# Kernel tuning notes

Hardware: AMD Instinct MI355X
Metric: run time of the kernel (lower is better)

The kernel has to match this reference:

```python
import jax, jax.numpy as jnp
import numpy as np

HEADS, DH, DIM = 16, 64, 1024
GAMMA, LAMBDA_REG = 0.01, 0.001


def _ln(x, g, b, eps=1e-5):
    mu = x.mean(-1, keepdims=True)
    var = x.var(-1, keepdims=True)  # biased var, matches torch LayerNorm
    return (x - mu) / jnp.sqrt(var + eps) * g + b


def setup_inputs() -> dict:
    key = jax.random.key(0)
    ks = jax.random.split(key, 8)
    B, NQ, NK = 8, 512, 512
    inner = HEADS * DH
    rn = lambda i, shp, sc: jax.random.normal(ks[i], shp, jnp.float32) * sc
    return {
        "q": rn(0, (B, NQ, DIM), 1.0),
        "k": rn(1, (B, NK, DIM), 1.0),
        "v": rn(2, (B, NK, DIM), 1.0),
        "ln_g": jnp.ones((DIM,), jnp.float32),
        "ln_b": jnp.zeros((DIM,), jnp.float32),
        "w_in": rn(3, (DIM, inner), 0.02),
        "wp_w1": rn(4, (2 * DH, DH), 0.05),
        "wp_b1": jnp.zeros((DH,), jnp.float32),
        "wp_lng": jnp.ones((DH,), jnp.float32),
        "wp_lnb": jnp.zeros((DH,), jnp.float32),
        "wp_w2": rn(5, (DH, DH // 2), 0.05),
        "wp_b2": jnp.zeros((DH // 2,), jnp.float32),
        "wp_w3": rn(6, (DH // 2, 3), 0.05),
        "wp_b3": jnp.zeros((3,), jnp.float32),
        "w_temp": jnp.ones((1,), jnp.float32) * 0.8,
        "w_out": rn(7, (inner, DIM), 0.02),
        "b_out": jnp.zeros((DIM,), jnp.float32),
    }


def reference(q, k, v, ln_g, ln_b, w_in, wp_w1, wp_b1, wp_lng, wp_lnb,
              wp_w2, wp_b2, wp_w3, wp_b3, w_temp, w_out, b_out):
    sg = jax.lax.stop_gradient

    def proj(x):  # input_linear (dropout=identity in eval) + head split
        y = _ln(x, ln_g, ln_b) @ w_in                      # [B,N,inner]
        B, N, _ = y.shape
        return y.reshape(B, N, HEADS, DH).transpose(2, 0, 1, 3)  # [h,B,N,d]

    f_q, f_k, f_v = proj(q), proj(k), proj(v)
    m = f_k.shape[2]
    eps = 1e-8

    # --- cosine component (clamp applied twice, as in source) ---
    dots = jnp.einsum('hbnd,hbmd->hbnm', f_q, f_k)
    n1 = jnp.linalg.norm(f_q, axis=-1, keepdims=True) + eps   # [h,B,Nq,1]
    n2 = jnp.linalg.norm(f_k, axis=-1, keepdims=True) + eps   # [h,B,Nk,1]
    cosine_sim = jnp.clip(dots / (n1 * jnp.swapaxes(n2, -1, -2)), -0.98, 0.98)

    # --- regularized covariance component ---
    f_kc = f_k - f_k.mean(axis=2, keepdims=True)
    f_qc = f_q - f_q.mean(axis=-1, keepdims=True)
    cov = jnp.einsum('hbnd,hbmd->hbnm', f_qc, f_kc) / (DH ** 0.5 + 1e-6)
    health = jnp.std(cov, ddof=1)
    base = LAMBDA_REG / max(m, 1)
    reg = jnp.where(health < 1e-5, base * 5.0,
                    jnp.where(health < 1e-3, base * 2.0, base))
    cov = jnp.clip(reg * cov, -25.0, 25.0)

    # --- margin-based variance component (eval: adaptive_gamma = gamma) ---
    fqn = f_q / jnp.maximum(jnp.linalg.norm(f_q, axis=-1, keepdims=True), 1e-6)
    fkn = f_k / jnp.maximum(jnp.linalg.norm(f_k, axis=-1, keepdims=True), 1e-6)
    cs = jnp.clip(jnp.einsum('hbnd,hbmd->hbnm', fqn, fkn), -0.98, 0.98)
    margin = jnp.clip(GAMMA - cs, 0.0, 5.0)
    var_c = jnp.broadcast_to(margin.mean(-1, keepdims=True), cs.shape)

    # --- dynamic per-head weight predictor MLP ---
    qk = jnp.concatenate([f_q.mean(axis=(1, 2)), f_k.mean(axis=(1, 2))], -1)  # [h,2d]
    h1 = jax.nn.relu(_ln(qk @ wp_w1 + wp_b1, wp_lng, wp_lnb))
    h2 = jax.nn.relu(h1 @ wp_w2 + wp_b2)
    logits = jax.nn.softmax(h2 @ wp_w3 + wp_b3, -1)  # MLP ends in Softmax
    temp = jnp.clip(w_temp, 0.1, 5.0)
    w = jax.nn.softmax(logits / temp, -1)            # second softmax with temp
    w = jnp.clip(w, 0.08, 0.75)
    w = w / w.sum(-1, keepdims=True)
    cw = w[:, 0].reshape(HEADS, 1, 1, 1)
    covw = w[:, 1].reshape(HEADS, 1, 1, 1)
    varw = w[:, 2].reshape(HEADS, 1, 1, 1)

    # --- health-based normalization (stds detached, as in source) ---
    cn = sg(jnp.std(cosine_sim, ddof=1)) + 1e-6
    covn = sg(jnp.std(cov, ddof=1)) + 1e-6
    varn = sg(jnp.std(var_c, ddof=1)) + 1e-6
    ch = jnp.minimum(cn, 1.0)
    covh = jnp.minimum(covn * 10.0, 1.0)
    varh = jnp.minimum(varn * 10.0, 1.0)
    dots_f = (cw * (cosine_sim / cn * ch)
              + covw * (cov / covn * 0.4 * covh)
              + varw * (var_c / varn * 0.4 * varh))

    # --- diversity-adaptive softmax temperature ---
    div = jnp.std(dots_f, ddof=1)
    atemp = jnp.where(div < 1e-5, 0.05, jnp.where(div < 1e-3, 0.2, 0.5 + div))
    atemp = jnp.clip(atemp, 0.05, 2.0)
    attn = jax.nn.softmax(dots_f / atemp, axis=-1)

    out = jnp.einsum('hbnm,hbmd->hbnd', attn, f_v)
    out = out.transpose(1, 2, 0, 3).reshape(q.shape[0], q.shape[1], HEADS * DH)
    return out @ w_out + b_out  # output_linear (dropout=identity)
```

## Files before the change

kernel.cpp:

```cpp
#include <hip/hip_runtime.h>
#include <math.h>

#define NHEADS 16
#define DHEAD  64
#define NDIM   1024
#define NB     8
#define NSEQ   512
#define NROWS  4096
#define NHB    128
#define NTOTD  33554432.0

typedef __bf16 bf16x8 __attribute__((ext_vector_type(8)));
typedef __bf16 bf16x4 __attribute__((ext_vector_type(4)));
typedef float  f32x4  __attribute__((ext_vector_type(4)));

#define MFMA(a,b,c) __builtin_amdgcn_mfma_f32_16x16x32_bf16(a,b,c,0,0,0)

static __device__ __forceinline__ size_t qk_off(int hbq, int n, int d){
  return ((size_t)hbq*32 + (n>>4))*1024 + (size_t)(d>>3)*128 + (size_t)(n&15)*8 + (d&7);
}
static __device__ __forceinline__ size_t fr_off(int r, int k2, int kblocks8){
  return ((size_t)(r>>4)*kblocks8 + (k2>>3))*128 + (size_t)(r&15)*8 + (k2&7);
}

#define O_DSUMH  0
#define O_DSUME  1024
#define O_SCAL   2048
#define O_COEF   3072
#define O_W      4096
#define O_RQ1    131072
#define O_RQ2    393216
#define O_MQ     655360
#define O_QDMK   917504
#define O_RK1    1179648
#define O_RK2    1441792
#define O_KS2    1703936
#define O_MARG   1966080
#define O_RCS    2228224
#define O_RCOV   2490368
#define O_MK     2752512
#define O_QCOL   2785280
#define O_QHI    4194304
#define O_QLO    12582912
#define O_KHI    20971520
#define O_KLO    29360128
#define O_VTH    37748736
#define O_VTL    46137344
#define O_LNST   54525952
#define O_WTH    71303168
#define O_WTL    73400320
#define O_OUTH   75497472
#define O_OUTL   83886080
#define O_WOTH   92274688
#define O_WOTL   94371840

static __device__ __forceinline__ float clamp98(float x){ return fminf(fmaxf(x,-0.98f),0.98f); }

__global__ __launch_bounds__(256) void ln_stats_kernel(const float* __restrict__ q,
    const float* __restrict__ k, const float* __restrict__ v, float* __restrict__ st){
  int row = blockIdx.x, t = threadIdx.x;
  const float* x = (blockIdx.y==0) ? q : (blockIdx.y==1 ? k : v);
  float4 vv = *(const float4*)(x + (size_t)row*1024 + t*4);
  float s  = vv.x+vv.y+vv.z+vv.w;
  float ss = vv.x*vv.x+vv.y*vv.y+vv.z*vv.z+vv.w*vv.w;
  for (int off=32; off; off>>=1){ s += __shfl_down(s,off); ss += __shfl_down(ss,off); }
  __shared__ float sh[8];
  if ((t&63)==0){ sh[t>>6]=s; sh[4+(t>>6)]=ss; }
  __syncthreads();
  if (t==0){
    float S=sh[0]+sh[1]+sh[2]+sh[3], SS=sh[4]+sh[5]+sh[6]+sh[7];
    float mu = S*(1.0f/1024.0f);
    st[blockIdx.y*8192 + row*2]   = mu;
    st[blockIdx.y*8192 + row*2+1] = 1.0f/sqrtf(SS*(1.0f/1024.0f) - mu*mu + 1e-5f);
  }
}

__global__ __launch_bounds__(256) void transpose_split_kernel(const float* __restrict__ wsrc,
    __bf16* __restrict__ th, __bf16* __restrict__ tl){
  __shared__ float tile[64][65];
  int k0 = blockIdx.x*64, n0 = blockIdx.y*64;
  int t = threadIdx.x;
  int c = t&63, r4 = t>>6;
  #pragma unroll
  for (int i=0;i<16;i++){
    int kr = r4 + i*4;
    tile[kr][c] = wsrc[(size_t)(k0+kr)*1024 + n0 + c];
  }
  __syncthreads();
  #pragma unroll
  for (int i=0;i<16;i++){
    int nr = r4 + i*4;
    float v = tile[c][nr];
    __bf16 hv = (__bf16)v;
    size_t o = fr_off(n0+nr, k0+c, 128);
    th[o] = hv; tl[o] = (__bf16)(v - (float)hv);
  }
}

__global__ __launch_bounds__(256,4) void proj_gemm_kernel(
  const float* __restrict__ q, const float* __restrict__ k, const float* __restrict__ v,
  const float* __restrict__ lnst0,
  const float* __restrict__ gv, const float* __restrict__ bv,
  const __bf16* __restrict__ Bth, const __bf16* __restrict__ Btl,
  __bf16* __restrict__ qhi, __bf16* __restrict__ qlo,
  __bf16* __restrict__ khi, __bf16* __restrict__ klo,
  __bf16* __restrict__ vth, __bf16* __restrict__ vtl)
{
  __shared__ __bf16 Ash[128][72];
  __shared__ __bf16 Asl[128][72];
  int z = blockIdx.z;
  const float* X = (z==0)? q : (z==1? k : v);
  const float* lnst = lnst0 + z*8192;
  __bf16* oh = (z==0)? qhi : (z==1? khi : vth);
  __bf16* ol = (z==0)? qlo : (z==1? klo : vtl);
  int t = threadIdx.x, w = t>>6, lane = t&63, lr = lane&15, lq = lane>>4;
  int vid = blockIdx.y*16 + blockIdx.x;
  int cX = vid&7, r2 = vid>>3;
  int ytile = cX*4 + (r2>>4);
  int xtile = r2&15;
  int rbase = ytile*128;
  int cbase = xtile*64;
  int wr = w>>1, wc = w&1;
  int srow = t>>3;
  int scol = (t&7)*8;
  int cb16_0 = (cbase + wc*32)>>4;
  f32x4 acc[4][2] = {};
  for (int kt=0; kt<16; kt++){
    int k0 = kt*64;
    bf16x8 va[4], vA[4];
    float4 g0 = *(const float4*)(gv + k0 + scol);
    float4 g1 = *(const float4*)(gv + k0 + scol + 4);
    float4 b0 = *(const float4*)(bv + k0 + scol);
    float4 b1 = *(const float4*)(bv + k0 + scol + 4);
    #pragma unroll
    for (int r=0;r<4;r++){
      int row = rbase + r*32 + srow;
      size_t gi = (size_t)row*1024 + k0 + scol;
      float4 x0 = *(const float4*)(X + gi);
      float4 x1 = *(const float4*)(X + gi + 4);
      float mu = lnst[row*2], rs = lnst[row*2+1];
      float o[8];
      o[0]=(x0.x-mu)*rs*g0.x+b0.x; o[1]=(x0.y-mu)*rs*g0.y+b0.y;
      o[2]=(x0.z-mu)*rs*g0.z+b0.z; o[3]=(x0.w-mu)*rs*g0.w+b0.w;
      o[4]=(x1.x-mu)*rs*g1.x+b1.x; o[5]=(x1.y-mu)*rs*g1.y+b1.y;
      o[6]=(x1.z-mu)*rs*g1.z+b1.z; o[7]=(x1.w-mu)*rs*g1.w+b1.w;
      bf16x8 hv, lv;
      #pragma unroll
      for (int e=0;e<8;e++){
        __bf16 hb_ = (__bf16)o[e];
        hv[e] = hb_; lv[e] = (__bf16)(o[e]-(float)hb_);
      }
      va[r]=hv; vA[r]=lv;
    }
    #pragma unroll
    for (int r=0;r<4;r++){
      *(bf16x8*)&Ash[r*32+srow][scol] = va[r];
      *(bf16x8*)&Asl[r*32+srow][scol] = vA[r];
    }
    __syncthreads();
    #pragma unroll
    for (int kc=0; kc<2; kc++){
      int ko = kc*32 + lq*8;
      bf16x8 ah[4], al[4], bh[2], bl[2];
      #pragma unroll
      for (int i=0;i<4;i++){
        ah[i] = *(const bf16x8*)&Ash[wr*64 + i*16 + lr][ko];
        al[i] = *(const bf16x8*)&Asl[wr*64 + i*16 + lr][ko];
      }
      #pragma unroll
      for (int j=0;j<2;j++){
        size_t bo = ((size_t)(cb16_0+j)*128 + (k0>>3) + kc*4)*128 + (size_t)lane*8;
        bh[j] = *(const bf16x8*)(Bth + bo);
        bl[j] = *(const bf16x8*)(Btl + bo);
      }
      #pragma unroll
      for (int i=0;i<4;i++)
        #pragma unroll
        for (int j=0;j<2;j++){
          acc[i][j] = MFMA(al[i], bh[j], acc[i][j]);
          acc[i][j] = MFMA(ah[i], bl[j], acc[i][j]);
          acc[i][j] = MFMA(ah[i], bh[j], acc[i][j]);
        }
    }
    __syncthreads();
  }
  #pragma unroll
  for (int i=0;i<4;i++)
    #pragma unroll
    for (int j=0;j<2;j++)
      #pragma unroll
      for (int r=0;r<4;r++){
        int row = rbase + wr*64 + i*16 + lq*4 + r;
        int col = cbase + wc*32 + j*16 + lr;
        float val = acc[i][j][r];
        __bf16 hv = (__bf16)val;
        __bf16 lv = (__bf16)(val - (float)hv);
        int n = row & 511, b2 = row >> 9;
        int hh = col >> 6, d = col & 63;
        int hbq = hh*8 + b2;
        size_t o;
        if (z<2){
          o = qk_off(hbq, n, d);
        } else {
          o = (((size_t)hbq*4 + (d>>4))*16 + (n>>5))*512
            + (size_t)((((n>>3)&3)*16) + (d&15))*8 + (n&7);
        }
        oh[o] = hv; ol[o] = lv;
      }
}

__global__ __launch_bounds__(256) void final_gemm_kernel(
  const __bf16* __restrict__ Ah, const __bf16* __restrict__ Al,
  const __bf16* __restrict__ Bth, const __bf16* __restrict__ Btl,
  const float* __restrict__ bias, float* __restrict__ of)
{
  int t = threadIdx.x, w = t>>6, lane = t&63, lr = lane&15, lq = lane>>4;
  int vid = blockIdx.y*16 + blockIdx.x;
  int cX = vid&7, r2 = vid>>3;
  int ytile = cX*4 + (r2>>4);
  int xtile = r2&15;
  int rbase = ytile*128;
  int cbase = xtile*64;
  int wr = w>>1, wc = w&1;
  int rb16_0 = (rbase + wr*64)>>4;
  int cb16_0 = (cbase + wc*32)>>4;
  f32x4 acc[4][2] = {};
  for (int ks=0; ks<32; ks++){
    int kb = ks*4;
    bf16x8 ah[4], al[4], bh[2], bl[2];
    #pragma unroll
    for (int i=0;i<4;i++){
      size_t ao = ((size_t)(rb16_0+i)*128 + kb)*128 + (size_t)lane*8;
      ah[i] = *(const bf16x8*)(Ah + ao);
      al[i] = *(const bf16x8*)(Al + ao);
    }
    #pragma unroll
    for (int j=0;j<2;j++){
      size_t bo = ((size_t)(cb16_0+j)*128 + kb)*128 + (size_t)lane*8;
      bh[j] = *(const bf16x8*)(Bth + bo);
      bl[j] = *(const bf16x8*)(Btl + bo);
    }
    #pragma unroll
    for (int i=0;i<4;i++)
      #pragma unroll
      for (int j=0;j<2;j++){
        acc[i][j] = MFMA(al[i], bh[j], acc[i][j]);
        acc[i][j] = MFMA(ah[i], bl[j], acc[i][j]);
        acc[i][j] = MFMA(ah[i], bh[j], acc[i][j]);
      }
  }
  #pragma unroll
  for (int i=0;i<4;i++)
    #pragma unroll
    for (int j=0;j<2;j++)
      #pragma unroll
      for (int r=0;r<4;r++){
        int row = rbase + wr*64 + i*16 + lq*4 + r;
        int col = cbase + wc*32 + j*16 + lr;
        of[(size_t)row*1024 + col] = acc[i][j][r] + bias[col];
      }
}

__global__ void kstats_kernel(const __bf16* __restrict__ kh, const __bf16* __restrict__ kl,
    float* __restrict__ mk, float* __restrict__ rk1, float* __restrict__ rk2, float* __restrict__ ks2){
  int hb = blockIdx.x;
  size_t base = (size_t)hb*32768;
  int t = threadIdx.x;
  __shared__ float csA[32][64];
  __shared__ float mks_lds[64];
  __shared__ float mksum_sh;
  int c2 = t&7, mg = t>>3;
  float fs[8] = {};
  for (int m=mg; m<512; m+=32){
    size_t off = base + (size_t)(m>>4)*1024 + c2*128 + (size_t)(m&15)*8;
    bf16x8 h = *(const bf16x8*)(kh+off);
    bf16x8 l = *(const bf16x8*)(kl+off);
    #pragma unroll
    for (int e=0;e<8;e++) fs[e] += (float)h[e]+(float)l[e];
  }
  #pragma unroll
  for (int e=0;e<8;e++) csA[mg][c2*8+e] = fs[e];
  __syncthreads();
  if (t<64){
    float s=0;
    #pragma unroll
    for (int g=0;g<32;g++) s += csA[g][t];
    float vv = s*(1.0f/512.0f);
    mk[hb*64+t] = vv;
    mks_lds[t] = vv;
  }
  __syncthreads();
  if (t==0){
    float s=0;
    for (int i=0;i<64;i++) s += mks_lds[i];
    mksum_sh = s;
  }
  __syncthreads();
  float mks = mksum_sh;
  int l8 = t&7, rg = t>>3;
  for (int m=rg; m<512; m+=32){
    size_t off = base + (size_t)(m>>4)*1024 + l8*128 + (size_t)(m&15)*8;
    bf16x8 h = *(const bf16x8*)(kh+off);
    bf16x8 l = *(const bf16x8*)(kl+off);
    float s=0, ss=0;
    #pragma unroll
    for (int e=0;e<8;e++){ float vv=(float)h[e]+(float)l[e]; s+=vv; ss+=vv*vv; }
    for (int o2=4;o2;o2>>=1){ s+=__shfl_xor(s,o2); ss+=__shfl_xor(ss,o2); }
    if (l8==0){
      float nk = sqrtf(ss);
      rk1[hb*512+m] = 1.0f/(nk+1e-8f);
      rk2[hb*512+m] = 1.0f/fmaxf(nk,1e-6f);
      ks2[hb*512+m] = s - mks;
    }
  }
}

__global__ void qstats_kernel(const __bf16* __restrict__ qh, const __bf16* __restrict__ ql,
    const float* __restrict__ mk, float* __restrict__ rq1, float* __restrict__ rq2,
    float* __restrict__ mq, float* __restrict__ qdotmk, float* __restrict__ qcol){
  int hb = blockIdx.x;
  size_t base = (size_t)hb*32768;
  int t = threadIdx.x;
  __shared__ float csA[32][64];
  __shared__ float mks_lds[64];
  int c2 = t&7, mg = t>>3;
  if (t<64) mks_lds[t] = mk[hb*64+t];
  float fs[8] = {};
  for (int m=mg; m<512; m+=32){
    size_t off = base + (size_t)(m>>4)*1024 + c2*128 + (size_t)(m&15)*8;
    bf16x8 h = *(const bf16x8*)(qh+off);
    bf16x8 l = *(const bf16x8*)(ql+off);
    #pragma unroll
    for (int e=0;e<8;e++) fs[e] += (float)h[e]+(float)l[e];
  }
  #pragma unroll
  for (int e=0;e<8;e++) csA[mg][c2*8+e] = fs[e];
  __syncthreads();
  if (t<64){
    float s=0;
    #pragma unroll
    for (int g=0;g<32;g++) s += csA[g][t];
    qcol[hb*64+t] = s;
  }
  int l8 = t&7, rg = t>>3;
  float mkv[8];
  #pragma unroll
  for (int e=0;e<8;e++) mkv[e] = mks_lds[l8*8+e];
  for (int n=rg; n<512; n+=32){
    size_t off = base + (size_t)(n>>4)*1024 + l8*128 + (size_t)(n&15)*8;
    bf16x8 h = *(const bf16x8*)(qh+off);
    bf16x8 l = *(const bf16x8*)(ql+off);
    float s=0, ss=0, qd=0;
    #pragma unroll
    for (int e=0;e<8;e++){
      float vv=(float)h[e]+(float)l[e];
      s+=vv; ss+=vv*vv; qd+=vv*mkv[e];
    }
    for (int o2=4;o2;o2>>=1){ s+=__shfl_xor(s,o2); ss+=__shfl_xor(ss,o2); qd+=__shfl_xor(qd,o2); }
    if (l8==0){
      float nq = sqrtf(ss);
      rq1[hb*512+n] = 1.0f/(nq+1e-8f);
      rq2[hb*512+n] = 1.0f/fmaxf(nq,1e-6f);
      mq[hb*512+n]  = s*(1.0f/64.0f);
      qdotmk[hb*512+n] = qd;
    }
  }
}

__global__ void mlp_kernel(const float* __restrict__ qcol, const float* __restrict__ mk,
   const float* __restrict__ w1, const float* __restrict__ b1, const float* __restrict__ lng,
   const float* __restrict__ lnb, const float* __restrict__ w2, const float* __restrict__ b2,
   const float* __restrict__ w3, const float* __restrict__ b3, const float* __restrict__ wtemp,
   float* __restrict__ W){
  int h = blockIdx.x;
  int j = threadIdx.x;
  __shared__ float qk[128], h1[64], h2[32];
  float sq=0, sk=0;
  #pragma unroll
  for (int b=0;b<8;b++){
    sq += qcol[(h*8+b)*64 + j];
    sk += mk[(h*8+b)*64 + j];
  }
  qk[j]    = sq*(1.0f/4096.0f);
  qk[64+j] = sk*(1.0f/8.0f);
  __syncthreads();
  float a = b1[j];
  for (int i=0;i<128;i++) a += qk[i]*w1[i*64+j];
  float s=a, ss=a*a;
  for (int off=32; off; off>>=1){ s += __shfl_xor(s,off); ss += __shfl_xor(ss,off); }
  float mu = s*(1.0f/64.0f), var = ss*(1.0f/64.0f)-mu*mu;
  float v = (a-mu)/sqrtf(var+1e-5f)*lng[j] + lnb[j];
  h1[j] = fmaxf(v, 0.0f);
  __syncthreads();
  if (j<32){
    float a2 = b2[j];
    for (int i=0;i<64;i++) a2 += h1[i]*w2[i*32+j];
    h2[j] = fmaxf(a2,0.0f);
  }
  __syncthreads();
  if (j==0){
    float l[3];
    for (int kq=0;kq<3;kq++){ float a3=b3[kq]; for(int i=0;i<32;i++) a3 += h2[i]*w3[i*3+kq]; l[kq]=a3; }
    float m = fmaxf(l[0],fmaxf(l[1],l[2]));
    float e0=expf(l[0]-m), e1=expf(l[1]-m), e2=expf(l[2]-m);
    float si = 1.0f/(e0+e1+e2);
    float temp = fminf(fmaxf(wtemp[0], 0.1f), 5.0f);
    float t0=e0*si/temp, t1=e1*si/temp, t2=e2*si/temp;
    float m2 = fmaxf(t0,fmaxf(t1,t2));
    float f0=expf(t0-m2), f1=expf(t1-m2), f2=expf(t2-m2);
    float s2i = 1.0f/(f0+f1+f2);
    float wv[3] = {f0*s2i, f1*s2i, f2*s2i};
    float wsum=0.0f;
    for (int kq=0;kq<3;kq++){ wv[kq]=fminf(fmaxf(wv[kq],0.08f),0.75f); wsum+=wv[kq]; }
    for (int kq=0;kq<3;kq++) W[h*3+kq] = wv[kq]/wsum;
  }
}

__global__ __launch_bounds__(256) void s1_mfma_kernel(
  const __bf16* __restrict__ qhp, const __bf16* __restrict__ qlp,
  const __bf16* __restrict__ khp, const __bf16* __restrict__ klp,
  const float* __restrict__ rq1, const float* __restrict__ rq2,
  const float* __restrict__ mq, const float* __restrict__ qdmk,
  const float* __restrict__ rk1, const float* __restrict__ rk2,
  const float* __restrict__ ks2,
  double* __restrict__ dsumH, float* __restrict__ margin,
  float* __restrict__ rcs, float* __restrict__ rcov)
{
  int vid = blockIdx.y*4 + blockIdx.x;
  int cX = vid&7, r2 = vid>>3;
  int hb = cX*16 + (r2>>2);
  int n0 = (r2&3)*128;
  size_t qb = (size_t)hb*32768;
  __shared__ float sm[512][3];
  __shared__ float sn[128][4];
  int t = threadIdx.x;
  for (int mm=t; mm<512; mm+=256){
    int m = hb*512 + mm;
    sm[mm][0]=rk1[m]; sm[mm][1]=rk2[m]; sm[mm][2]=ks2[m];
  }
  if (t<128){
    int n = hb*512 + n0 + t;
    sn[t][0]=rq1[n]; sn[t][1]=rq2[n]; sn[t][2]=mq[n]; sn[t][3]=qdmk[n];
  }
  __syncthreads();
  int w = t>>6, lane = t&63, lr = lane&15, lq = lane>>4;
  int nw = w*32;
  float lcs=0,lcs2=0,lcov=0,lcov2=0,lcscov=0;
  float mrow[2][4]={}, csr[2][4]={}, cvr[2][4]={};
  for (int mc=0; mc<4; mc++){
    int m0 = mc*128;
    f32x4 acc[2][8] = {};
    #pragma unroll
    for (int kc=0; kc<2; kc++){
      bf16x8 ah[2], al[2];
      #pragma unroll
      for (int i=0;i<2;i++){
        size_t off = qb + (size_t)(((n0+nw)>>4)+i)*1024 + kc*512 + (size_t)lane*8;
        ah[i] = *(const bf16x8*)(qhp + off);
        al[i] = *(const bf16x8*)(qlp + off);
      }
      #pragma unroll
      for (int j=0;j<8;j++){
        size_t off = qb + (size_t)((m0>>4)+j)*1024 + kc*512 + (size_t)lane*8;
        bf16x8 bh = *(const bf16x8*)(khp + off);
        bf16x8 bl = *(const bf16x8*)(klp + off);
        #pragma unroll
        for (int i=0;i<2;i++){
          acc[i][j] = MFMA(ah[i], bh, acc[i][j]);
          acc[i][j] = MFMA(ah[i], bl, acc[i][j]);
          acc[i][j] = MFMA(al[i], bh, acc[i][j]);
        }
      }
    }
    #pragma unroll
    for (int i=0;i<2;i++){
      float nr1[4],nr2[4],nmq[4],nqd[4];
      #pragma unroll
      for (int r=0;r<4;r++){
        int nl = nw + i*16 + lq*4 + r;
        nr1[r]=sn[nl][0]; nr2[r]=sn[nl][1]; nmq[r]=sn[nl][2]; nqd[r]=sn[nl][3];
      }
      #pragma unroll
      for (int j=0;j<8;j++){
        int ml = m0 + j*16 + lr;
        float k1=sm[ml][0], k2=sm[ml][1], ksv=sm[ml][2];
        #pragma unroll
        for (int r=0;r<4;r++){
          float dv = acc[i][j][r];
          float cs = clamp98(dv*nr1[r]*k1);
          float c2 = clamp98(dv*nr2[r]*k2);
          float mg = fminf(fmaxf(0.01f-c2,0.0f),5.0f);
          float cv = dv - nqd[r] - nmq[r]*ksv;
          lcs+=cs; lcs2+=cs*cs; lcov+=cv; lcov2+=cv*cv; lcscov+=cs*cv;
          mrow[i][r]+=mg; csr[i][r]+=cs; cvr[i][r]+=cv;
        }
      }
    }
  }
  for (int off=1; off<16; off<<=1)
    #pragma unroll
    for (int i=0;i<2;i++)
      #pragma unroll
      for (int r=0;r<4;r++){
        mrow[i][r]+=__shfl_xor(mrow[i][r],off);
        csr[i][r] +=__shfl_xor(csr[i][r],off);
        cvr[i][r]+=__shfl_xor(cvr[i][r],off);
      }
  if (lr==0){
    #pragma unroll
    for (int i=0;i<2;i++)
      #pragma unroll
      for (int r=0;r<4;r++){
        int n = hb*512 + n0 + nw + i*16 + lq*4 + r;
        margin[n] = mrow[i][r]*(1.0f/512.0f);
        rcs[n]    = csr[i][r];
        rcov[n]   = cvr[i][r];
      }
  }
  for (int off=32; off; off>>=1){
    lcs+=__shfl_xor(lcs,off); lcs2+=__shfl_xor(lcs2,off);
    lcov+=__shfl_xor(lcov,off); lcov2+=__shfl_xor(lcov2,off);
    lcscov+=__shfl_xor(lcscov,off);
  }
  __shared__ double red[4][5];
  if (lane==0){ red[w][0]=lcs; red[w][1]=lcs2; red[w][2]=lcov; red[w][3]=lcov2; red[w][4]=lcscov; }
  __syncthreads();
  if (t==0){
    int h = hb>>3;
    for (int c=0;c<5;c++)
      atomicAdd(&dsumH[h*5+c], red[0][c]+red[1][c]+red[2][c]+red[3][c]);
  }
}

__global__ void margfin_kernel(const float* __restrict__ margin, double* __restrict__ dsumE){
  double s=0, ss=0;
  for (int k2=0;k2<4;k2++){
    int idx = blockIdx.x*1024 + k2*256 + threadIdx.x;
    float v = margin[idx];
    s += v; ss += (double)v*v;
  }
  for (int off=32; off; off>>=1){ s+=__shfl_down(s,off); ss+=__shfl_down(ss,off); }
  __shared__ double sh[8];
  int t = threadIdx.x;
  if ((t&63)==0){ sh[t>>6]=s; sh[4+(t>>6)]=ss; }
  __syncthreads();
  if (t==0){
    atomicAdd(dsumE+0, sh[0]+sh[1]+sh[2]+sh[3]);
    atomicAdd(dsumE+1, sh[4]+sh[5]+sh[6]+sh[7]);
  }
}

__global__ void scalars1_kernel(const double* __restrict__ dsumH, double* __restrict__ dsumE,
                                const float* __restrict__ W, float* __restrict__ coef){
  double Scs=0,Scs2=0,Scov=0,Scov2=0;
  for (int h=0;h<16;h++){
    Scs += dsumH[h*5+0]; Scs2 += dsumH[h*5+1];
    Scov += dsumH[h*5+2]; Scov2 += dsumH[h*5+3];
  }
  double N = NTOTD;
  double cn = sqrt(fmax((Scs2-Scs*Scs/N)/(N-1.0),0.0)) + 1e-6;
  double ch = fmin(cn, 1.0);
  const double covscale = 1.0/8.000001;
  double sc_ = Scov*covscale, sc2_ = Scov2*covscale*covscale;
  double health = sqrt(fmax((sc2_-sc_*sc_/N)/(N-1.0),0.0));
  double base = 0.001/512.0;
  double reg = health<1e-5 ? base*5.0 : (health<1e-3 ? base*2.0 : base);
  double covn = reg*health + 1e-6;
  double covh = fmin(covn*10.0, 1.0);
  double vs = dsumE[0]*512.0, vs2 = dsumE[1]*512.0;
  double varn = sqrt(fmax((vs2 - vs*vs/N)/(N-1.0),0.0)) + 1e-6;
  double varh = fmin(varn*10.0, 1.0);
  double sdf=0, sdf2=0;
  for (int h=0;h<16;h++){
    double cC  = (double)W[h*3+0]*ch/cn;
    double cCv = (double)W[h*3+1]*reg*covscale*0.4*covh/covn;
    double cVr = (double)W[h*3+2]*0.4*varh/varn;
    coef[h*3+0] = (float)cC;
    coef[h*3+1] = (float)cCv;
    coef[h*3+2] = (float)cVr;
    sdf  += cC*dsumH[h*5+0] + cCv*dsumH[h*5+2];
    sdf2 += cC*cC*dsumH[h*5+1] + cCv*cCv*dsumH[h*5+3] + 2.0*cC*cCv*dsumH[h*5+4];
  }
  dsumE[2] = sdf;
  dsumE[3] = sdf2;
}

__global__ void rowfold_kernel(const float* __restrict__ margin, const float* __restrict__ rcs,
                               const float* __restrict__ rcov, const float* __restrict__ coef,
                               double* __restrict__ dsumE){
  int idx = blockIdx.x*256 + threadIdx.x;
  int h = idx >> 12;
  float cC = coef[h*3+0], cCv = coef[h*3+1], cVr = coef[h*3+2];
  float vc = cVr * margin[idx];
  double s0 = 512.0*(double)vc;
  double s1 = 2.0*(double)vc*((double)cC*(double)rcs[idx] + (double)cCv*(double)rcov[idx])
            + 512.0*(double)vc*(double)vc;
  for (int off=32; off; off>>=1){ s0+=__shfl_down(s0,off); s1+=__shfl_down(s1,off); }
  __shared__ double sh[8];
  int t = threadIdx.x;
  if ((t&63)==0){ sh[t>>6]=s0; sh[4+(t>>6)]=s1; }
  __syncthreads();
  if (t==0){
    atomicAdd(dsumE+2, sh[0]+sh[1]+sh[2]+sh[3]);
    atomicAdd(dsumE+3, sh[4]+sh[5]+sh[6]+sh[7]);
  }
}

__global__ void scalars2_kernel(const double* __restrict__ dsumE, float* __restrict__ scal){
  double N = NTOTD;
  double div = sqrt(fmax((dsumE[3]-dsumE[2]*dsumE[2]/N)/(N-1.0),0.0));
  double at = div<1e-5 ? 0.05 : (div<1e-3 ? 0.2 : 0.5+div);
  at = fmin(fmax(at,0.05),2.0);
  scal[0] = (float)(1.0/at);
}

#define PSTRIDE 536
__global__ __launch_bounds__(512) void s3_mfma_kernel(
  const __bf16* __restrict__ qhp, const __bf16* __restrict__ qlp,
  const __bf16* __restrict__ khp, const __bf16* __restrict__ klp,
  const __bf16* __restrict__ vth, const __bf16* __restrict__ vtl,
  const float* __restrict__ rq1, const float* __restrict__ mq,
  const float* __restrict__ qdmk, const float* __restrict__ rk1,
  const float* __restrict__ ks2, const float* __restrict__ margin,
  const float* __restrict__ coef, const float* __restrict__ scal,
  __bf16* __restrict__ outh, __bf16* __restrict__ outl)
{
  int vid = blockIdx.y*16 + blockIdx.x;
  int cX = vid&7, r2 = vid>>3;
  int hb = cX*16 + (r2>>4);
  int n0 = (r2&15)*32;
  int h = hb>>3, b = hb&7;
  size_t qb = (size_t)hb*32768;

  __shared__ unsigned short Plds[32][PSTRIDE];
  __shared__ float nst[32][4];
  __shared__ float mst[512][2];
  __shared__ float pmax[32][8];
  __shared__ float psum[32][8];

  int t = threadIdx.x, w = t>>6, lane = t&63, lr = lane&15, lq = lane>>4;
  if (t<32){
    int n = hb*512 + n0 + t;
    nst[t][0] = rq1[n]; nst[t][1] = mq[n]; nst[t][2] = qdmk[n];
    nst[t][3] = coef[h*3+2]*margin[n];
  }
  {
    int m = hb*512 + t;
    mst[t][0] = rk1[m]; mst[t][1] = ks2[m];
  }
  float cC = coef[h*3+0], cCv = coef[h*3+1];
  float invat = scal[0];
  __syncthreads();

  int ms0 = w*64;
  f32x4 acc[2][4] = {};
  #pragma unroll
  for (int kc=0; kc<2; kc++){
    bf16x8 qhf[2], qlf[2];
    #pragma unroll
    for (int i=0;i<2;i++){
      size_t off = qb + (size_t)((n0>>4)+i)*1024 + kc*512 + (size_t)lane*8;
      qhf[i] = *(const bf16x8*)(qhp + off);
      qlf[i] = *(const bf16x8*)(qlp + off);
    }
    #pragma unroll
    for (int j=0;j<4;j++){
      size_t off = qb + (size_t)((ms0>>4)+j)*1024 + kc*512 + (size_t)lane*8;
      bf16x8 khf = *(const bf16x8*)(khp + off);
      bf16x8 klf = *(const bf16x8*)(klp + off);
      #pragma unroll
      for (int i=0;i<2;i++){
        acc[i][j] = MFMA(qlf[i], khf, acc[i][j]);
        acc[i][j] = MFMA(qhf[i], klf, acc[i][j]);
        acc[i][j] = MFMA(qhf[i], khf, acc[i][j]);
      }
    }
  }
  float rmax[2][4];
  #pragma unroll
  for (int i=0;i<2;i++){
    float a0[4],a1[4],a2[4],a3[4];
    #pragma unroll
    for (int r=0;r<4;r++){
      int nl = i*16 + lq*4 + r;
      a0[r]=nst[nl][0]; a1[r]=nst[nl][1]; a2[r]=nst[nl][2]; a3[r]=nst[nl][3];
      rmax[i][r] = -1e30f;
    }
    #pragma unroll
    for (int j=0;j<4;j++){
      int m = ms0 + j*16 + lr;
      float k1 = mst[m][0], ksv = mst[m][1];
      #pragma unroll
      for (int r=0;r<4;r++){
        float dv = acc[i][j][r];
        float cs = clamp98(dv*a0[r]*k1);
        float covr = dv - a2[r] - a1[r]*ksv;
        float df = cC*cs + cCv*covr + a3[r];
        acc[i][j][r] = df;
        rmax[i][r] = fmaxf(rmax[i][r], df);
      }
    }
  }
  #pragma unroll
  for (int i=0;i<2;i++)
    #pragma unroll
    for (int r=0;r<4;r++)
      for (int off=1; off<16; off<<=1)
        rmax[i][r] = fmaxf(rmax[i][r], __shfl_xor(rmax[i][r], off));
  if (lr==0){
    #pragma unroll
    for (int i=0;i<2;i++)
      #pragma unroll
      for (int r=0;r<4;r++)
        pmax[i*16+lq*4+r][w] = rmax[i][r];
  }
  __syncthreads();
  float rsum[2][4] = {};
  #pragma unroll
  for (int i=0;i<2;i++){
    float Mf[4];
    #pragma unroll
    for (int r=0;r<4;r++){
      int nl = i*16+lq*4+r;
      float m0_ = fmaxf(fmaxf(pmax[nl][0],pmax[nl][1]),fmaxf(pmax[nl][2],pmax[nl][3]));
      float m1_ = fmaxf(fmaxf(pmax[nl][4],pmax[nl][5]),fmaxf(pmax[nl][6],pmax[nl][7]));
      Mf[r] = fmaxf(m0_,m1_);
    }
    #pragma unroll
    for (int j=0;j<4;j++){
      int m = ms0 + j*16 + lr;
      #pragma unroll
      for (int r=0;r<4;r++){
        float p = __expf((acc[i][j][r]-Mf[r])*invat);
        rsum[i][r] += p;
        *(__bf16*)&Plds[i*16+lq*4+r][m] = (__bf16)p;
      }
    }
  }
  #pragma unroll
  for (int i=0;i<2;i++)
    #pragma unroll
    for (int r=0;r<4;r++)
      for (int off=1; off<16; off<<=1)
        rsum[i][r] += __shfl_xor(rsum[i][r], off);
  if (lr==0){
    #pragma unroll
    for (int i=0;i<2;i++)
      #pragma unroll
      for (int r=0;r<4;r++)
        psum[i*16+lq*4+r][w] = rsum[i][r];
  }
  __syncthreads();

  int rt = (w&1)*16;
  int dtg = w>>1;
  f32x4 acc2 = {};
  for (int kc=0; kc<16; kc++){
    bf16x8 pa = *(const bf16x8*)&Plds[rt+lr][kc*32 + lq*8];
    size_t vi = (((size_t)hb*4 + dtg)*16 + kc)*512 + (size_t)lane*8;
    bf16x8 vh = *(const bf16x8*)(vth + vi);
    bf16x8 vl = *(const bf16x8*)(vtl + vi);
    acc2 = MFMA(pa, vl, acc2);
    acc2 = MFMA(pa, vh, acc2);
  }
  float rsinv[4];
  #pragma unroll
  for (int r=0;r<4;r++){
    int nl = rt + lq*4 + r;
    float s0_ = psum[nl][0]+psum[nl][1]+psum[nl][2]+psum[nl][3];
    float s1_ = psum[nl][4]+psum[nl][5]+psum[nl][6]+psum[nl][7];
    rsinv[r] = 1.0f/(s0_+s1_);
  }
  #pragma unroll
  for (int r=0;r<4;r++){
    float o = acc2[r]*rsinv[r];
    int rowg = b*512 + n0 + rt + lq*4 + r;
    int colg = h*64 + dtg*16 + lr;
    size_t oi = fr_off(rowg, colg, 128);
    __bf16 hv = (__bf16)o;
    outh[oi] = hv;
    outl[oi] = (__bf16)(o - (float)hv);
  }
}

extern "C" void kernel_launch(void* const* d_in, const int* in_sizes, int n_in,
                              void* d_out, int out_size, void* d_ws, size_t ws_size,
                              hipStream_t stream) {
  (void)in_sizes; (void)n_in; (void)out_size; (void)ws_size;
  const float* q     = (const float*)d_in[0];
  const float* k     = (const float*)d_in[1];
  const float* v     = (const float*)d_in[2];
  const float* ln_g  = (const float*)d_in[3];
  const float* ln_b  = (const float*)d_in[4];
  const float* w_in  = (const float*)d_in[5];
  const float* wp_w1 = (const float*)d_in[6];
  const float* wp_b1 = (const float*)d_in[7];
  const float* wp_lng= (const float*)d_in[8];
  const float* wp_lnb= (const float*)d_in[9];
  const float* wp_w2 = (const float*)d_in[10];
  const float* wp_b2 = (const float*)d_in[11];
  const float* wp_w3 = (const float*)d_in[12];
  const float* wp_b3 = (const float*)d_in[13];
  const float* w_temp= (const float*)d_in[14];
  const float* w_out = (const float*)d_in[15];
  const float* b_out = (const float*)d_in[16];

  char* ws = (char*)d_ws;
  double* dsumH = (double*)(ws + O_DSUMH);
  double* dsumE = (double*)(ws + O_DSUME);
  float* scal  = (float*)(ws + O_SCAL);
  float* coef  = (float*)(ws + O_COEF);
  float* W     = (float*)(ws + O_W);
  float* rq1   = (float*)(ws + O_RQ1);
  float* rq2   = (float*)(ws + O_RQ2);
  float* mqp   = (float*)(ws + O_MQ);
  float* qdmk  = (float*)(ws + O_QDMK);
  float* rk1   = (float*)(ws + O_RK1);
  float* rk2   = (float*)(ws + O_RK2);
  float* ks2   = (float*)(ws + O_KS2);
  float* marg  = (float*)(ws + O_MARG);
  float* rcs   = (float*)(ws + O_RCS);
  float* rcov  = (float*)(ws + O_RCOV);
  float* mk    = (float*)(ws + O_MK);
  float* qcol  = (float*)(ws + O_QCOL);
  float* lnst  = (float*)(ws + O_LNST);
  __bf16* qhi  = (__bf16*)(ws + O_QHI);
  __bf16* qlo  = (__bf16*)(ws + O_QLO);
  __bf16* khi  = (__bf16*)(ws + O_KHI);
  __bf16* klo  = (__bf16*)(ws + O_KLO);
  __bf16* vth  = (__bf16*)(ws + O_VTH);
  __bf16* vtl  = (__bf16*)(ws + O_VTL);
  __bf16* wth  = (__bf16*)(ws + O_WTH);
  __bf16* wtl  = (__bf16*)(ws + O_WTL);
  __bf16* outh = (__bf16*)(ws + O_OUTH);
  __bf16* outl = (__bf16*)(ws + O_OUTL);
  __bf16* woth = (__bf16*)(ws + O_WOTH);
  __bf16* wotl = (__bf16*)(ws + O_WOTL);
  float* outf  = (float*)d_out;

  hipMemsetAsync(ws + O_DSUMH, 0, 2048, stream);

  transpose_split_kernel<<<dim3(16,16),256,0,stream>>>(w_in,  wth, wtl);
  transpose_split_kernel<<<dim3(16,16),256,0,stream>>>(w_out, woth, wotl);
  ln_stats_kernel<<<dim3(4096,3),256,0,stream>>>(q, k, v, lnst);

  proj_gemm_kernel<<<dim3(16,32,3),256,0,stream>>>(q, k, v, lnst, ln_g, ln_b, wth, wtl,
                                                   qhi, qlo, khi, klo, vth, vtl);

  kstats_kernel<<<128,256,0,stream>>>(khi, klo, mk, rk1, rk2, ks2);
  qstats_kernel<<<128,256,0,stream>>>(qhi, qlo, mk, rq1, rq2, mqp, qdmk, qcol);
  mlp_kernel<<<16,64,0,stream>>>(qcol,mk,wp_w1,wp_b1,wp_lng,wp_lnb,wp_w2,wp_b2,wp_w3,wp_b3,w_temp,W);

  s1_mfma_kernel<<<dim3(4,128),256,0,stream>>>(qhi,qlo,khi,klo,rq1,rq2,mqp,qdmk,rk1,rk2,ks2,
                                               dsumH,marg,rcs,rcov);
  margfin_kernel<<<64,256,0,stream>>>(marg, dsumE);
  scalars1_kernel<<<1,1,0,stream>>>(dsumH, dsumE, W, coef);
  rowfold_kernel<<<256,256,0,stream>>>(marg, rcs, rcov, coef, dsumE);
  scalars2_kernel<<<1,1,0,stream>>>(dsumE, scal);

  s3_mfma_kernel<<<dim3(16,128),512,0,stream>>>(qhi,qlo,khi,klo,vth,vtl,
                                                rq1,mqp,qdmk,rk1,ks2,marg,coef,scal,outh,outl);
  final_gemm_kernel<<<dim3(16,32),256,0,stream>>>(outh, outl, woth, wotl, b_out, outf);
}
```

Before: 358.0 us.

## Precompute LayerNorm bf16 hi/lo fragments and stream them directly into projection GEMM

LayerNorm and the bf16 hi/lo split of q, k and v now run in a separate kernel that writes MFMA-fragment-ordered buffers. The projection GEMM then loads A fragments straight from global memory with no LDS staging or block barriers. It runs as three sequential launches per input, reusing a single scratch buffer, instead of one fused launch over all three inputs. This removes the shared-memory round trip and the redundant per-tile normalization inside the GEMM. The cost is an extra write and read of the normalized activations, less overlap between the three inputs, and no LDS reuse of A across waves.

```diff
diff --git a/kernel.cpp b/kernel.cpp
--- a/kernel.cpp
+++ b/kernel.cpp
@@ -28,6 +28,7 @@
 #define O_SCAL   2048
 #define O_COEF   3072
 #define O_W      4096
+#define O_LNST   16384
 #define O_RQ1    131072
 #define O_RQ2    393216
 #define O_MQ     655360
@@ -46,7 +47,8 @@
 #define O_KLO    29360128
 #define O_VTH    37748736
 #define O_VTL    46137344
-#define O_LNST   54525952
+#define O_LNFH   54525952
+#define O_LNFL   62914560
 #define O_WTH    71303168
 #define O_WTL    73400320
 #define O_OUTH   75497472
@@ -75,6 +77,49 @@
   }
 }
 
+__global__ __launch_bounds__(256) void ln_split_frag_kernel(const float* __restrict__ X,
+    const float* __restrict__ lnst, const float* __restrict__ gv, const float* __restrict__ bv,
+    __bf16* __restrict__ oh, __bf16* __restrict__ ol){
+  __shared__ __bf16 sh[16][256];
+  __shared__ __bf16 sl[16][256];
+  int rb = blockIdx.x;
+  int t = threadIdx.x;
+  int r = t>>4, c16 = (t&15)*16;
+  int row = rb*16 + r;
+  float mu = lnst[row*2], rs = lnst[row*2+1];
+  size_t xbase = (size_t)row*1024;
+  int kb = t>>3;
+  int rr = (t*2)&15;
+  for (int ch=0; ch<4; ch++){
+    int c0 = ch*256;
+    #pragma unroll
+    for (int q4=0; q4<4; q4++){
+      int col = c0 + c16 + q4*4;
+      float4 xv = *(const float4*)(X + xbase + col);
+      float4 g  = *(const float4*)(gv + col);
+      float4 b  = *(const float4*)(bv + col);
+      float o0 = (xv.x-mu)*rs*g.x + b.x;
+      float o1 = (xv.y-mu)*rs*g.y + b.y;
+      float o2 = (xv.z-mu)*rs*g.z + b.z;
+      float o3 = (xv.w-mu)*rs*g.w + b.w;
+      bf16x4 hv, lv;
+      hv[0]=(__bf16)o0; lv[0]=(__bf16)(o0-(float)hv[0]);
+      hv[1]=(__bf16)o1; lv[1]=(__bf16)(o1-(float)hv[1]);
+      hv[2]=(__bf16)o2; lv[2]=(__bf16)(o2-(float)hv[2]);
+      hv[3]=(__bf16)o3; lv[3]=(__bf16)(o3-(float)hv[3]);
+      *(bf16x4*)&sh[r][c16 + q4*4] = hv;
+      *(bf16x4*)&sl[r][c16 + q4*4] = lv;
+    }
+    __syncthreads();
+    size_t base = ((size_t)rb*128 + (c0>>3))*128;
+    *(bf16x8*)(oh + base + (size_t)kb*128 + rr*8)     = *(bf16x8*)&sh[rr][kb*8];
+    *(bf16x8*)(oh + base + (size_t)kb*128 + (rr+1)*8) = *(bf16x8*)&sh[rr+1][kb*8];
+    *(bf16x8*)(ol + base + (size_t)kb*128 + rr*8)     = *(bf16x8*)&sl[rr][kb*8];
+    *(bf16x8*)(ol + base + (size_t)kb*128 + (rr+1)*8) = *(bf16x8*)&sl[rr+1][kb*8];
+    __syncthreads();
+  }
+}
+
 __global__ __launch_bounds__(256) void transpose_split_kernel(const float* __restrict__ wsrc,
     __bf16* __restrict__ th, __bf16* __restrict__ tl){
   __shared__ float tile[64][65];
@@ -97,22 +142,12 @@
   }
 }
 
-__global__ __launch_bounds__(256,4) void proj_gemm_kernel(
-  const float* __restrict__ q, const float* __restrict__ k, const float* __restrict__ v,
-  const float* __restrict__ lnst0,
-  const float* __restrict__ gv, const float* __restrict__ bv,
+template<int LAYOUT>
+__global__ __launch_bounds__(256) void proj_frag_kernel(
+  const __bf16* __restrict__ Ah, const __bf16* __restrict__ Al,
   const __bf16* __restrict__ Bth, const __bf16* __restrict__ Btl,
-  __bf16* __restrict__ qhi, __bf16* __restrict__ qlo,
-  __bf16* __restrict__ khi, __bf16* __restrict__ klo,
-  __bf16* __restrict__ vth, __bf16* __restrict__ vtl)
+  __bf16* __restrict__ oh, __bf16* __restrict__ ol)
 {
-  __shared__ __bf16 Ash[128][72];
-  __shared__ __bf16 Asl[128][72];
-  int z = blockIdx.z;
-  const float* X = (z==0)? q : (z==1? k : v);
-  const float* lnst = lnst0 + z*8192;
-  __bf16* oh = (z==0)? qhi : (z==1? khi : vth);
-  __bf16* ol = (z==0)? qlo : (z==1? klo : vtl);
   int t = threadIdx.x, w = t>>6, lane = t&63, lr = lane&15, lq = lane>>4;
   int vid = blockIdx.y*16 + blockIdx.x;
   int cX = vid&7, r2 = vid>>3;
@@ -121,68 +156,32 @@
   int rbase = ytile*128;
   int cbase = xtile*64;
   int wr = w>>1, wc = w&1;
-  int srow = t>>3;
-  int scol = (t&7)*8;
+  int rb16_0 = (rbase + wr*64)>>4;
   int cb16_0 = (cbase + wc*32)>>4;
   f32x4 acc[4][2] = {};
-  for (int kt=0; kt<16; kt++){
-    int k0 = kt*64;
-    bf16x8 va[4], vA[4];
-    float4 g0 = *(const float4*)(gv + k0 + scol);
-    float4 g1 = *(const float4*)(gv + k0 + scol + 4);
-    float4 b0 = *(const float4*)(bv + k0 + scol);
-    float4 b1 = *(const float4*)(bv + k0 + scol + 4);
-    #pragma unroll
-    for (int r=0;r<4;r++){
-      int row = rbase + r*32 + srow;
-      size_t gi = (size_t)row*1024 + k0 + scol;
-      float4 x0 = *(const float4*)(X + gi);
-      float4 x1 = *(const float4*)(X + gi + 4);
-      float mu = lnst[row*2], rs = lnst[row*2+1];
-      float o[8];
-      o[0]=(x0.x-mu)*rs*g0.x+b0.x; o[1]=(x0.y-mu)*rs*g0.y+b0.y;
-      o[2]=(x0.z-mu)*rs*g0.z+b0.z; o[3]=(x0.w-mu)*rs*g0.w+b0.w;
-      o[4]=(x1.x-mu)*rs*g1.x+b1.x; o[5]=(x1.y-mu)*rs*g1.y+b1.y;
-      o[6]=(x1.z-mu)*rs*g1.z+b1.z; o[7]=(x1.w-mu)*rs*g1.w+b1.w;
-      bf16x8 hv, lv;
-      #pragma unroll
-      for (int e=0;e<8;e++){
-        __bf16 hb_ = (__bf16)o[e];
-        hv[e] = hb_; lv[e] = (__bf16)(o[e]-(float)hb_);
-      }
-      va[r]=hv; vA[r]=lv;
-    }
-    #pragma unroll
-    for (int r=0;r<4;r++){
-      *(bf16x8*)&Ash[r*32+srow][scol] = va[r];
-      *(bf16x8*)&Asl[r*32+srow][scol] = vA[r];
-    }
-    __syncthreads();
-    #pragma unroll
-    for (int kc=0; kc<2; kc++){
-      int ko = kc*32 + lq*8;
-      bf16x8 ah[4], al[4], bh[2], bl[2];
-      #pragma unroll
-      for (int i=0;i<4;i++){
-        ah[i] = *(const bf16x8*)&Ash[wr*64 + i*16 + lr][ko];
-        al[i] = *(const bf16x8*)&Asl[wr*64 + i*16 + lr][ko];
-      }
+  for (int ks=0; ks<32; ks++){
+    int kb = ks*4;
+    bf16x8 ah[4], al[4], bh[2], bl[2];
+    #pragma unroll
+    for (int i=0;i<4;i++){
+      size_t ao = ((size_t)(rb16_0+i)*128 + kb)*128 + (size_t)lane*8;
+      ah[i] = *(const bf16x8*)(Ah + ao);
+      al[i] = *(const bf16x8*)(Al + ao);
+    }
+    #pragma unroll
+    for (int j=0;j<2;j++){
+      size_t bo = ((size_t)(cb16_0+j)*128 + kb)*128 + (size_t)lane*8;
+      bh[j] = *(const bf16x8*)(Bth + bo);
+      bl[j] = *(const bf16x8*)(Btl + bo);
+    }
+    #pragma unroll
+    for (int i=0;i<4;i++)
       #pragma unroll
       for (int j=0;j<2;j++){
-        size_t bo = ((size_t)(cb16_0+j)*128 + (k0>>3) + kc*4)*128 + (size_t)lane*8;
-        bh[j] = *(const bf16x8*)(Bth + bo);
-        bl[j] = *(const bf16x8*)(Btl + bo);
-      }
-      #pragma unroll
-      for (int i=0;i<4;i++)
-        #pragma unroll
-        for (int j=0;j<2;j++){
-          acc[i][j] = MFMA(al[i], bh[j], acc[i][j]);
-          acc[i][j] = MFMA(ah[i], bl[j], acc[i][j]);
-          acc[i][j] = MFMA(ah[i], bh[j], acc[i][j]);
-        }
-    }
-    __syncthreads();
+        acc[i][j] = MFMA(al[i], bh[j], acc[i][j]);
+        acc[i][j] = MFMA(ah[i], bl[j], acc[i][j]);
+        acc[i][j] = MFMA(ah[i], bh[j], acc[i][j]);
+      }
   }
   #pragma unroll
   for (int i=0;i<4;i++)
@@ -199,7 +198,7 @@
         int hh = col >> 6, d = col & 63;
         int hbq = hh*8 + b2;
         size_t o;
-        if (z<2){
+        if (LAYOUT==0){
           o = qk_off(hbq, n, d);
         } else {
           o = (((size_t)hbq*4 + (d>>4))*16 + (n>>5))*512
@@ -811,6 +810,7 @@
   float* scal  = (float*)(ws + O_SCAL);
   float* coef  = (float*)(ws + O_COEF);
   float* W     = (float*)(ws + O_W);
+  float* lnst  = (float*)(ws + O_LNST);
   float* rq1   = (float*)(ws + O_RQ1);
   float* rq2   = (float*)(ws + O_RQ2);
   float* mqp   = (float*)(ws + O_MQ);
@@ -823,13 +823,14 @@
   float* rcov  = (float*)(ws + O_RCOV);
   float* mk    = (float*)(ws + O_MK);
   float* qcol  = (float*)(ws + O_QCOL);
-  float* lnst  = (float*)(ws + O_LNST);
   __bf16* qhi  = (__bf16*)(ws + O_QHI);
   __bf16* qlo  = (__bf16*)(ws + O_QLO);
   __bf16* khi  = (__bf16*)(ws + O_KHI);
   __bf16* klo  = (__bf16*)(ws + O_KLO);
   __bf16* vth  = (__bf16*)(ws + O_VTH);
   __bf16* vtl  = (__bf16*)(ws + O_VTL);
+  __bf16* lnfh = (__bf16*)(ws + O_LNFH);
+  __bf16* lnfl = (__bf16*)(ws + O_LNFL);
   __bf16* wth  = (__bf16*)(ws + O_WTH);
   __bf16* wtl  = (__bf16*)(ws + O_WTL);
   __bf16* outh = (__bf16*)(ws + O_OUTH);
@@ -844,8 +845,12 @@
   transpose_split_kernel<<<dim3(16,16),256,0,stream>>>(w_out, woth, wotl);
   ln_stats_kernel<<<dim3(4096,3),256,0,stream>>>(q, k, v, lnst);
 
-  proj_gemm_kernel<<<dim3(16,32,3),256,0,stream>>>(q, k, v, lnst, ln_g, ln_b, wth, wtl,
-                                                   qhi, qlo, khi, klo, vth, vtl);
+  ln_split_frag_kernel<<<256,256,0,stream>>>(q, lnst,        ln_g, ln_b, lnfh, lnfl);
+  proj_frag_kernel<0><<<dim3(16,32),256,0,stream>>>(lnfh, lnfl, wth, wtl, qhi, qlo);
+  ln_split_frag_kernel<<<256,256,0,stream>>>(k, lnst+8192,   ln_g, ln_b, lnfh, lnfl);
+  proj_frag_kernel<0><<<dim3(16,32),256,0,stream>>>(lnfh, lnfl, wth, wtl, khi, klo);
+  ln_split_frag_kernel<<<256,256,0,stream>>>(v, lnst+16384,  ln_g, ln_b, lnfh, lnfl);
+  proj_frag_kernel<1><<<dim3(16,32),256,0,stream>>>(lnfh, lnfl, wth, wtl, vth, vtl);
 
   kstats_kernel<<<128,256,0,stream>>>(khi, klo, mk, rk1, rk2, ks2);
   qstats_kernel<<<128,256,0,stream>>>(qhi, qlo, mk, rq1, rq2, mqp, qdmk, qcol);
```

After: 388.2 us. 8.4% more time.
